# Performance work log

Hardware: AMD Instinct MI355X
Metric: run time of the kernel (lower is better)

Reference implementation:

```python
import jax, jax.numpy as jnp
import numpy as np

_SQRT4PI = float(np.sqrt(4.0 * np.pi))

def spherical_harmonics_l2(vec):
    # e3nn real spherical harmonics, lmax=2, normalize=True, normalization='integral'
    # component-normalized values divided by sqrt(4*pi); e3nn (x,y,z) ordering with y as zenith
    r = jnp.linalg.norm(vec, axis=-1, keepdims=True)
    u = vec / jnp.maximum(r, 1e-12)
    x, y, z = u[..., 0], u[..., 1], u[..., 2]
    c1 = np.float32(np.sqrt(3.0)); c2 = np.float32(np.sqrt(15.0)); c3 = np.float32(np.sqrt(5.0))
    sh = jnp.stack([
        jnp.ones_like(x),                      # l=0
        c1 * x, c1 * y, c1 * z,                # l=1
        c2 * x * z,                            # l=2
        c2 * x * y,
        c3 * (y * y - 0.5 * (x * x + z * z)),
        c2 * y * z,
        (c2 * 0.5) * (z * z - x * x),
    ], axis=-1)
    return sh * np.float32(1.0 / _SQRT4PI)

def setup_inputs() -> dict:
    key = jax.random.key(0)
    ks = jax.random.split(key, 8)
    N, M, C, F, SH = 50000, 12, 128, 64, 9
    return dict(
        atom_fea=jax.random.normal(ks[0], (N, C), jnp.float32),
        nbr_fea=jax.random.normal(ks[1], (N, M, F), jnp.float32),
        nbr_idx=jax.random.randint(ks[2], (N, M), 0, N),
        pos=jax.random.normal(ks[3], (N, 3), jnp.float32),
        w1=jax.random.normal(ks[4], (F, F), jnp.float32) * np.float32(1.0 / np.sqrt(F)),
        b1=jnp.zeros((F,), jnp.float32),
        w2=jax.random.normal(ks[5], (F, SH), jnp.float32) * np.float32(1.0 / np.sqrt(F)),
        b2=jnp.zeros((SH,), jnp.float32),
        tp_w=jax.random.normal(ks[6], (C, C), jnp.float32),  # FCTP weight, path (Cx0e)x(1x0e)->(Cx0e)
        bn_gamma=jnp.ones((C,), jnp.float32),
        bn_beta=jnp.zeros((C,), jnp.float32),
    )

def reference(atom_fea, nbr_fea, nbr_idx, pos, w1, b1, w2, b2, tp_w, bn_gamma, bn_beta):
    N, M, F = nbr_fea.shape
    C = atom_fea.shape[1]
    src = nbr_idx.reshape(-1)                                  # (E,)
    h_j = atom_fea[src]                                        # (E, C) gather
    # radial MLP: Linear -> Softplus -> Linear
    R = jax.nn.softplus(nbr_fea.reshape(N * M, F) @ w1 + b1) @ w2 + b2   # (E, 9)
    rel = pos[src] - jnp.repeat(pos, M, axis=0)                # (E, 3), dst = arange(N) repeated M times
    Y = spherical_harmonics_l2(rel)                            # (E, 9)
    W = R * Y                                                  # (E, 9)
    # FullyConnectedTensorProduct(Cx0e, 0e+1o+2e, Cx0e): only 0e x 0e -> 0e path survives,
    # fan-in normalization alpha = 1/sqrt(C)
    msg = (h_j @ tp_w) * W[:, :1] * np.float32(1.0 / np.sqrt(C))  # (E, C)
    # scatter-mean over dst: dst rows are contiguous blocks of size M per node
    agg = msg.reshape(N, M, C).mean(axis=1)                    # (N, C)
    x = atom_fea + agg
    # BatchNorm1d (training-mode batch statistics, eps=1e-5)
    mean = x.mean(axis=0)
    var = x.var(axis=0)
    xn = (x - mean) * jax.lax.rsqrt(var + 1e-5)
    return jax.nn.softplus(bn_gamma * xn + bn_beta)
```

## Files before the change

kernel.cpp:

```cpp
#include <hip/hip_runtime.h>
#include <hip/hip_bf16.h>
#include <cstddef>

#define N_NODES 50000
#define M_NBR   12
#define C_CH    128
#define F_DIM   64
#define E_EDGES (N_NODES * M_NBR)
#define NSUP    18750
#define SUP_PER_WAVE 4
#define NBLK_A  1172
#define NBLK_Y  782
#define NBLK_G  782

constexpr float SCALE_CE =
    (float)(1.0 / (3.5449077018110318 * 11.313708498984761 * 12.0));

typedef __bf16 bf16x8 __attribute__((ext_vector_type(8)));
typedef float  f32x4  __attribute__((ext_vector_type(4)));

__device__ __forceinline__ float softplus_f(float x) {
    const float t = __builtin_amdgcn_exp2f(-fabsf(x) * 1.44269504f);
    return fmaxf(x, 0.0f) + 0.69314718f * __builtin_amdgcn_logf(1.0f + t);
}

__device__ __forceinline__ float bfhi_to_f(unsigned int p) {
    return __uint_as_float(p & 0xffff0000u);
}
__device__ __forceinline__ float bflo_to_f(unsigned int p) {
    return __uint_as_float(p << 16);
}

__global__ __launch_bounds__(512) void kW(
    const float* __restrict__ w1,
    const float* __restrict__ tp_w,
    __bf16* __restrict__ fragW1,
    __bf16* __restrict__ fragTP)
{
    const int t = threadIdx.x;
    if (blockIdx.x == 0) {
        const int lane = t & 63;
        const int f = t >> 6;
        const int n = f >> 1, ks = f & 1;
        const int col16 = lane & 15, kgrp = lane >> 4;
        bf16x8 v;
        #pragma unroll
        for (int j = 0; j < 8; ++j)
            v[j] = (__bf16)w1[(ks * 32 + kgrp * 8 + j) * F_DIM + 16 * n + col16];
        *(bf16x8*)&fragW1[(size_t)t * 8] = v;
    } else {
        const int fid = (blockIdx.x - 1) * 512 + t;
        const int lane = fid & 63;
        const int f = fid >> 6;
        const int n = f >> 2, ks = f & 3;
        const int col16 = lane & 15, kgrp = lane >> 4;
        bf16x8 v;
        #pragma unroll
        for (int j = 0; j < 8; ++j)
            v[j] = (__bf16)tp_w[(ks * 32 + kgrp * 8 + j) * C_CH + 16 * n + col16];
        *(bf16x8*)&fragTP[(size_t)fid * 8] = v;
    }
}

__global__ __launch_bounds__(256) void kFront(
    const float* __restrict__ nbr_fea,
    const __bf16* __restrict__ fragW1,
    const float* __restrict__ b1,
    const float* __restrict__ w2,
    const float* __restrict__ b2,
    const float* __restrict__ atom_fea,
    const __bf16* __restrict__ fragTP,
    float* __restrict__ ce,
    __bf16* __restrict__ y)
{
    __shared__ __align__(16) unsigned char smem[18432];
    const int tid   = threadIdx.x;
    const int lane  = tid & 63;
    const int wid   = tid >> 6;
    const int col16 = lane & 15;
    const int kgrp  = lane >> 4;

    if (blockIdx.x < NBLK_A) {
        bf16x8 bfrag[4][2];
        #pragma unroll
        for (int f = 0; f < 8; ++f)
            bfrag[f >> 1][f & 1] = *(const bf16x8*)&fragW1[((size_t)f * 64 + lane) * 8];

        float b1v[4], w2v[4];
        #pragma unroll
        for (int n = 0; n < 4; ++n) {
            b1v[n] = b1[16 * n + col16];
            w2v[n] = w2[(16 * n + col16) * 9];
        }
        const float b2_0 = b2[0];

        __bf16* S = (__bf16*)(smem + (size_t)wid * 4608);
        const int sup_base = (blockIdx.x * 4 + wid) * SUP_PER_WAVE;

        float4 pre[8];
        if (sup_base < NSUP) {
            const float* g = nbr_fea + (size_t)sup_base * 32 * F_DIM;
            #pragma unroll
            for (int i = 0; i < 8; ++i)
                pre[i] = *(const float4*)(g + (size_t)(i * 64 + lane) * 4);
        }

        #pragma unroll
        for (int st = 0; st < SUP_PER_WAVE; ++st) {
            const int sup = sup_base + st;
            if (sup >= NSUP) break;

            #pragma unroll
            for (int i = 0; i < 8; ++i) {
                const int gi16 = i * 64 + lane;
                const int row = gi16 >> 4, u = gi16 & 15;
                union { __bf16 h[4]; uint2 u2; } pk;
                pk.h[0] = (__bf16)pre[i].x; pk.h[1] = (__bf16)pre[i].y;
                pk.h[2] = (__bf16)pre[i].z; pk.h[3] = (__bf16)pre[i].w;
                *(uint2*)&S[row * 72 + u * 4] = pk.u2;
            }
            if (st + 1 < SUP_PER_WAVE && sup + 1 < NSUP) {
                const float* g = nbr_fea + (size_t)(sup + 1) * 32 * F_DIM;
                #pragma unroll
                for (int i = 0; i < 8; ++i)
                    pre[i] = *(const float4*)(g + (size_t)(i * 64 + lane) * 4);
            }

            const long e0 = (long)sup * 32;
            #pragma unroll
            for (int t = 0; t < 2; ++t) {
                bf16x8 afrag[2];
                #pragma unroll
                for (int ks = 0; ks < 2; ++ks)
                    afrag[ks] = *(const bf16x8*)
                        &S[(t * 16 + col16) * 72 + ks * 32 + kgrp * 8];

                f32x4 acc[4];
                #pragma unroll
                for (int n = 0; n < 4; ++n) acc[n] = (f32x4){0.f, 0.f, 0.f, 0.f};
                #pragma unroll
                for (int ks = 0; ks < 2; ++ks)
                    #pragma unroll
                    for (int n = 0; n < 4; ++n)
                        acc[n] = __builtin_amdgcn_mfma_f32_16x16x32_bf16(
                            afrag[ks], bfrag[n][ks], acc[n], 0, 0, 0);

                float partial[4] = {0.f, 0.f, 0.f, 0.f};
                #pragma unroll
                for (int n = 0; n < 4; ++n)
                    #pragma unroll
                    for (int r = 0; r < 4; ++r) {
                        const float h = acc[n][r] + b1v[n];
                        partial[r] = fmaf(softplus_f(h), w2v[n], partial[r]);
                    }
                #pragma unroll
                for (int r = 0; r < 4; ++r) {
                    #pragma unroll
                    for (int off = 1; off <= 8; off <<= 1)
                        partial[r] += __shfl_xor(partial[r], off);
                }
                if (col16 == 0) {
                    const long et = e0 + t * 16;
                    #pragma unroll
                    for (int r = 0; r < 4; ++r)
                        ce[et + kgrp * 4 + r] = (partial[r] + b2_0) * SCALE_CE;
                }
            }
        }
    } else {
        __bf16* yl = (__bf16*)smem;
        const int blk  = blockIdx.x - NBLK_A;
        const int row  = blk * 64 + wid * 16 + col16;
        const int rowc = row < N_NODES ? row : N_NODES - 1;
        const float* ap = atom_fea + (size_t)rowc * C_CH + kgrp * 8;

        bf16x8 afrag[4];
        #pragma unroll
        for (int ks = 0; ks < 4; ++ks) {
            float4 f0 = *(const float4*)(ap + ks * 32);
            float4 f1 = *(const float4*)(ap + ks * 32 + 4);
            afrag[ks][0] = (__bf16)f0.x; afrag[ks][1] = (__bf16)f0.y;
            afrag[ks][2] = (__bf16)f0.z; afrag[ks][3] = (__bf16)f0.w;
            afrag[ks][4] = (__bf16)f1.x; afrag[ks][5] = (__bf16)f1.y;
            afrag[ks][6] = (__bf16)f1.z; afrag[ks][7] = (__bf16)f1.w;
        }

        #pragma unroll
        for (int n = 0; n < 8; ++n) {
            f32x4 acc = (f32x4){0.f, 0.f, 0.f, 0.f};
            #pragma unroll
            for (int ks = 0; ks < 4; ++ks) {
                bf16x8 bf = *(const bf16x8*)&fragTP[((size_t)(n * 4 + ks) * 64 + lane) * 8];
                acc = __builtin_amdgcn_mfma_f32_16x16x32_bf16(afrag[ks], bf, acc, 0, 0, 0);
            }
            #pragma unroll
            for (int r = 0; r < 4; ++r)
                yl[(wid * 16 + kgrp * 4 + r) * 136 + 16 * n + col16] = (__bf16)acc[r];
        }
        __syncthreads();

        #pragma unroll
        for (int it = 0; it < 4; ++it) {
            const int e  = it * 2048 + tid * 8;
            const int rw = e >> 7, cl = e & 127;
            const int grow = blk * 64 + rw;
            if (grow < N_NODES) {
                bf16x8 v = *(const bf16x8*)&yl[rw * 136 + cl];
                *(bf16x8*)&y[(size_t)grow * C_CH + cl] = v;
            }
        }
    }
}

__global__ __launch_bounds__(256, 6) void kG(
    const float* __restrict__ atom_fea,
    const __bf16* __restrict__ y,
    const int*   __restrict__ nbr_idx,
    const float* __restrict__ ce,
    unsigned int* __restrict__ xb,
    float* __restrict__ psum,
    float* __restrict__ psumsq)
{
    __shared__ float4 red[4][64];
    const int tid  = threadIdx.x;
    const int lane = tid & 63;
    const int wid  = tid >> 6;
    const int blk  = blockIdx.x;
    const int i0   = blk * 64 + wid * 16;

    float2 sum   = make_float2(0.f, 0.f);
    float2 sumsq = make_float2(0.f, 0.f);

    int   pidx = 0;
    float pce  = 0.f;
    if (i0 < N_NODES && lane < M_NBR) {
        pidx = nbr_idx[i0 * M_NBR + lane];
        pce  = ce[i0 * M_NBR + lane];
    }

    for (int t = 0; t < 16; ++t) {
        const int i = i0 + t;
        const int   cidx = pidx;
        const float cce  = pce;
        const int inext = i + 1;
        if (t < 15 && inext < N_NODES && lane < M_NBR) {
            pidx = nbr_idx[inext * M_NBR + lane];
            pce  = ce[inext * M_NBR + lane];
        }
        if (i < N_NODES) {
            float2 acc = make_float2(0.f, 0.f);
            #pragma unroll
            for (int m = 0; m < M_NBR; ++m) {
                const int   src = __shfl(cidx, m);
                const float c   = __shfl(cce, m);
                const unsigned int p =
                    *(const unsigned int*)(y + (size_t)src * C_CH + lane * 2);
                acc.x = fmaf(c, bflo_to_f(p), acc.x);
                acc.y = fmaf(c, bfhi_to_f(p), acc.y);
            }
            const float2 a = *(const float2*)(atom_fea + (size_t)i * C_CH + lane * 2);
            const float2 xv = make_float2(a.x + acc.x, a.y + acc.y);
            union { __bf16 h[2]; unsigned int u; } pk;
            pk.h[0] = (__bf16)xv.x;
            pk.h[1] = (__bf16)xv.y;
            xb[(size_t)i * 64 + lane] = pk.u;
            sum.x += xv.x; sum.y += xv.y;
            sumsq.x += xv.x * xv.x; sumsq.y += xv.y * xv.y;
        }
    }

    red[wid][lane] = make_float4(sum.x, sum.y, sumsq.x, sumsq.y);
    __syncthreads();
    if (tid < 128) {
        const int l = tid >> 1, comp = tid & 1;
        float s = 0.f, q = 0.f;
        #pragma unroll
        for (int w = 0; w < 4; ++w) {
            const float4 v = red[w][l];
            s += comp ? v.y : v.x;
            q += comp ? v.w : v.z;
        }
        psum[blk * 128 + tid]   = s;
        psumsq[blk * 128 + tid] = q;
    }
}

__global__ __launch_bounds__(1024) void kC1(
    const float* __restrict__ psum,
    const float* __restrict__ psumsq,
    float* __restrict__ mean_o,
    float* __restrict__ istd_o,
    int nblocks)
{
    __shared__ float red[2][8][128];
    const int t = threadIdx.x;
    const int c = t & 127;
    const int grp = t >> 7;
    float s = 0.f, ss = 0.f;
    for (int b = grp; b < nblocks; b += 8) {
        s  += psum[b * 128 + c];
        ss += psumsq[b * 128 + c];
    }
    red[0][grp][c] = s;
    red[1][grp][c] = ss;
    __syncthreads();
    if (t < 128) {
        float S = 0.f, SS = 0.f;
        #pragma unroll
        for (int k = 0; k < 8; ++k) { S += red[0][k][t]; SS += red[1][k][t]; }
        const float m   = S / (float)N_NODES;
        const float var = SS / (float)N_NODES - m * m;
        mean_o[t] = m;
        istd_o[t] = rsqrtf(var + 1e-5f);
    }
}

__global__ __launch_bounds__(256) void kC2(
    const unsigned int* __restrict__ xb,
    float* __restrict__ out,
    const float* __restrict__ mean_i,
    const float* __restrict__ istd_i,
    const float* __restrict__ gamma,
    const float* __restrict__ beta)
{
    __shared__ float sm[128], si[128], sg[128], sb[128];
    const int tid = threadIdx.x;
    if (tid < 128) {
        sm[tid] = mean_i[tid];
        si[tid] = istd_i[tid];
        sg[tid] = gamma[tid];
        sb[tid] = beta[tid];
    }
    __syncthreads();
    const size_t tix = (size_t)blockIdx.x * 256 + tid;
    const uint2 v = *(const uint2*)&xb[tix * 2];
    const int c0 = (int)(tix & 31) * 4;
    float r[4] = {bflo_to_f(v.x), bfhi_to_f(v.x), bflo_to_f(v.y), bfhi_to_f(v.y)};
    float4 o;
    #pragma unroll
    for (int t = 0; t < 4; ++t) {
        const int cc = c0 + t;
        const float xn = (r[t] - sm[cc]) * si[cc];
        r[t] = softplus_f(fmaf(sg[cc], xn, sb[cc]));
    }
    o.x = r[0]; o.y = r[1]; o.z = r[2]; o.w = r[3];
    *(float4*)&out[tix * 4] = o;
}

extern "C" void kernel_launch(void* const* d_in, const int* in_sizes, int n_in,
                              void* d_out, int out_size, void* d_ws, size_t ws_size,
                              hipStream_t stream)
{
    const float* atom_fea = (const float*)d_in[0];
    const float* nbr_fea  = (const float*)d_in[1];
    const int*   nbr_idx  = (const int*)d_in[2];
    const float* w1       = (const float*)d_in[4];
    const float* b1       = (const float*)d_in[5];
    const float* w2       = (const float*)d_in[6];
    const float* b2       = (const float*)d_in[7];
    const float* tp_w     = (const float*)d_in[8];
    const float* bn_gamma = (const float*)d_in[9];
    const float* bn_beta  = (const float*)d_in[10];

    float* out = (float*)d_out;
    float* ws  = (float*)d_ws;

    float* ce      = ws;
    float* psum    = ce + E_EDGES;
    float* psumsq  = psum + (size_t)NBLK_G * 128;
    float* mean_b  = psumsq + (size_t)NBLK_G * 128;
    float* istd_b  = mean_b + 128;
    __bf16* fragW1 = (__bf16*)(istd_b + 128);
    __bf16* fragTP = fragW1 + 4096;
    __bf16* ybuf   = fragTP + 16384;
    unsigned int* xbuf = (unsigned int*)(ybuf + 6400000);

    kW<<<5, 512, 0, stream>>>(w1, tp_w, fragW1, fragTP);
    kFront<<<NBLK_A + NBLK_Y, 256, 0, stream>>>(
        nbr_fea, fragW1, b1, w2, b2, atom_fea, fragTP, ce, ybuf);
    kG<<<NBLK_G, 256, 0, stream>>>(atom_fea, ybuf, nbr_idx, ce,
                                   xbuf, psum, psumsq);
    kC1<<<1, 1024, 0, stream>>>(psum, psumsq, mean_b, istd_b, NBLK_G);
    const int nC2 = (N_NODES * C_CH / 4) / 256;
    kC2<<<nC2, 256, 0, stream>>>(xbuf, out, mean_b, istd_b, bn_gamma, bn_beta);
}
```

Baseline: 110.0 us.

## Fold weight fragment packing into kFront via LDS and halve kG block size

Removes the separate kW launch that pre-packed w1 and tp_w into bf16 MFMA fragments. kFront blocks now stage the fp32 weights in shared memory and build the bf16 fragments themselves, with tp_w loaded one K-slice at a time. kG is also split into twice as many blocks, each covering 32 nodes instead of 64, to spread the gather across more workgroups. This saves one launch and its dependency, but every block now redoes the weight conversion and adds extra __syncthreads, and the BN partial-sum buffers double in size.

```diff
diff --git a/kernel.cpp b/kernel.cpp
--- a/kernel.cpp
+++ b/kernel.cpp
@@ -11,7 +11,7 @@
 #define SUP_PER_WAVE 4
 #define NBLK_A  1172
 #define NBLK_Y  782
-#define NBLK_G  782
+#define NBLK_G  1563
 
 constexpr float SCALE_CE =
     (float)(1.0 / (3.5449077018110318 * 11.313708498984761 * 12.0));
@@ -31,45 +31,14 @@
     return __uint_as_float(p << 16);
 }
 
-__global__ __launch_bounds__(512) void kW(
-    const float* __restrict__ w1,
-    const float* __restrict__ tp_w,
-    __bf16* __restrict__ fragW1,
-    __bf16* __restrict__ fragTP)
-{
-    const int t = threadIdx.x;
-    if (blockIdx.x == 0) {
-        const int lane = t & 63;
-        const int f = t >> 6;
-        const int n = f >> 1, ks = f & 1;
-        const int col16 = lane & 15, kgrp = lane >> 4;
-        bf16x8 v;
-        #pragma unroll
-        for (int j = 0; j < 8; ++j)
-            v[j] = (__bf16)w1[(ks * 32 + kgrp * 8 + j) * F_DIM + 16 * n + col16];
-        *(bf16x8*)&fragW1[(size_t)t * 8] = v;
-    } else {
-        const int fid = (blockIdx.x - 1) * 512 + t;
-        const int lane = fid & 63;
-        const int f = fid >> 6;
-        const int n = f >> 2, ks = f & 3;
-        const int col16 = lane & 15, kgrp = lane >> 4;
-        bf16x8 v;
-        #pragma unroll
-        for (int j = 0; j < 8; ++j)
-            v[j] = (__bf16)tp_w[(ks * 32 + kgrp * 8 + j) * C_CH + 16 * n + col16];
-        *(bf16x8*)&fragTP[(size_t)fid * 8] = v;
-    }
-}
-
 __global__ __launch_bounds__(256) void kFront(
     const float* __restrict__ nbr_fea,
-    const __bf16* __restrict__ fragW1,
+    const float* __restrict__ w1,
     const float* __restrict__ b1,
     const float* __restrict__ w2,
     const float* __restrict__ b2,
     const float* __restrict__ atom_fea,
-    const __bf16* __restrict__ fragTP,
+    const float* __restrict__ tp_w,
     float* __restrict__ ce,
     __bf16* __restrict__ y)
 {
@@ -81,10 +50,23 @@
     const int kgrp  = lane >> 4;
 
     if (blockIdx.x < NBLK_A) {
+        float* WS = (float*)smem;
+        #pragma unroll
+        for (int i = 0; i < 4; ++i) {
+            const int idx = (tid + i * 256) * 4;
+            *(float4*)&WS[idx] = *(const float4*)&w1[idx];
+        }
+        __syncthreads();
         bf16x8 bfrag[4][2];
         #pragma unroll
-        for (int f = 0; f < 8; ++f)
-            bfrag[f >> 1][f & 1] = *(const bf16x8*)&fragW1[((size_t)f * 64 + lane) * 8];
+        for (int n = 0; n < 4; ++n)
+            #pragma unroll
+            for (int ks = 0; ks < 2; ++ks)
+                #pragma unroll
+                for (int j = 0; j < 8; ++j)
+                    bfrag[n][ks][j] =
+                        (__bf16)WS[(ks * 32 + kgrp * 8 + j) * F_DIM + 16 * n + col16];
+        __syncthreads();
 
         float b1v[4], w2v[4];
         #pragma unroll
@@ -168,7 +150,6 @@
             }
         }
     } else {
-        __bf16* yl = (__bf16*)smem;
         const int blk  = blockIdx.x - NBLK_A;
         const int row  = blk * 64 + wid * 16 + col16;
         const int rowc = row < N_NODES ? row : N_NODES - 1;
@@ -185,18 +166,38 @@
             afrag[ks][6] = (__bf16)f1.z; afrag[ks][7] = (__bf16)f1.w;
         }
 
-        #pragma unroll
-        for (int n = 0; n < 8; ++n) {
-            f32x4 acc = (f32x4){0.f, 0.f, 0.f, 0.f};
-            #pragma unroll
-            for (int ks = 0; ks < 4; ++ks) {
-                bf16x8 bf = *(const bf16x8*)&fragTP[((size_t)(n * 4 + ks) * 64 + lane) * 8];
-                acc = __builtin_amdgcn_mfma_f32_16x16x32_bf16(afrag[ks], bf, acc, 0, 0, 0);
-            }
+        float* TS = (float*)smem;
+        f32x4 acc[8];
+        #pragma unroll
+        for (int n = 0; n < 8; ++n) acc[n] = (f32x4){0.f, 0.f, 0.f, 0.f};
+
+        #pragma unroll
+        for (int ks = 0; ks < 4; ++ks) {
+            const float* slice = tp_w + (size_t)ks * 32 * C_CH;
+            #pragma unroll
+            for (int i = 0; i < 4; ++i) {
+                const int idx = (tid + i * 256) * 4;
+                *(float4*)&TS[idx] = *(const float4*)&slice[idx];
+            }
+            __syncthreads();
+            #pragma unroll
+            for (int n = 0; n < 8; ++n) {
+                bf16x8 bf;
+                #pragma unroll
+                for (int j = 0; j < 8; ++j)
+                    bf[j] = (__bf16)TS[(kgrp * 8 + j) * C_CH + 16 * n + col16];
+                acc[n] = __builtin_amdgcn_mfma_f32_16x16x32_bf16(
+                    afrag[ks], bf, acc[n], 0, 0, 0);
+            }
+            __syncthreads();
+        }
+
+        __bf16* yl = (__bf16*)smem;
+        #pragma unroll
+        for (int n = 0; n < 8; ++n)
             #pragma unroll
             for (int r = 0; r < 4; ++r)
-                yl[(wid * 16 + kgrp * 4 + r) * 136 + 16 * n + col16] = (__bf16)acc[r];
-        }
+                yl[(wid * 16 + kgrp * 4 + r) * 136 + 16 * n + col16] = (__bf16)acc[n][r];
         __syncthreads();
 
         #pragma unroll
@@ -226,7 +227,7 @@
     const int lane = tid & 63;
     const int wid  = tid >> 6;
     const int blk  = blockIdx.x;
-    const int i0   = blk * 64 + wid * 16;
+    const int i0   = blk * 32 + wid * 8;
 
     float2 sum   = make_float2(0.f, 0.f);
     float2 sumsq = make_float2(0.f, 0.f);
@@ -238,12 +239,12 @@
         pce  = ce[i0 * M_NBR + lane];
     }
 
-    for (int t = 0; t < 16; ++t) {
+    for (int t = 0; t < 8; ++t) {
         const int i = i0 + t;
         const int   cidx = pidx;
         const float cce  = pce;
         const int inext = i + 1;
-        if (t < 15 && inext < N_NODES && lane < M_NBR) {
+        if (t < 7 && inext < N_NODES && lane < M_NBR) {
             pidx = nbr_idx[inext * M_NBR + lane];
             pce  = ce[inext * M_NBR + lane];
         }
@@ -370,14 +371,11 @@
     float* psumsq  = psum + (size_t)NBLK_G * 128;
     float* mean_b  = psumsq + (size_t)NBLK_G * 128;
     float* istd_b  = mean_b + 128;
-    __bf16* fragW1 = (__bf16*)(istd_b + 128);
-    __bf16* fragTP = fragW1 + 4096;
-    __bf16* ybuf   = fragTP + 16384;
+    __bf16* ybuf   = (__bf16*)(istd_b + 128);
     unsigned int* xbuf = (unsigned int*)(ybuf + 6400000);
 
-    kW<<<5, 512, 0, stream>>>(w1, tp_w, fragW1, fragTP);
     kFront<<<NBLK_A + NBLK_Y, 256, 0, stream>>>(
-        nbr_fea, fragW1, b1, w2, b2, atom_fea, fragTP, ce, ybuf);
+        nbr_fea, w1, b1, w2, b2, atom_fea, tp_w, ce, ybuf);
     kG<<<NBLK_G, 256, 0, stream>>>(atom_fea, ybuf, nbr_idx, ce,
                                    xbuf, psum, psumsq);
     kC1<<<1, 1024, 0, stream>>>(psum, psumsq, mean_b, istd_b, NBLK_G);
```

Measured after the change: 141.1 us. 1.28x slower.
